# Kernel tuning notes

Measured on AMD Instinct MI355X. Metric: run time of the kernel, lower is better.

## Reference

```python
import jax, jax.numpy as jnp
import numpy as np

N = 10000      # nodes
E = 640000     # directed edges
D = 128        # feature width
C = 10         # classes
G = 64         # graphs in batch


def setup_inputs() -> dict:
    key = jax.random.key(0)
    ks = jax.random.split(key, 9)
    x = jax.random.normal(ks[0], (N, D), dtype=jnp.float32)
    edge_index = jax.random.randint(ks[1], (2, E), 0, N, dtype=jnp.int64)
    batch = jnp.sort(jax.random.randint(ks[2], (N,), 0, G, dtype=jnp.int64))
    scale = 1.0 / np.sqrt(D)
    W1 = jax.random.normal(ks[3], (D, D), dtype=jnp.float32) * scale
    W2 = jax.random.normal(ks[4], (D, D), dtype=jnp.float32) * scale
    W3 = jax.random.normal(ks[5], (D, D), dtype=jnp.float32) * scale
    W4 = jax.random.normal(ks[6], (D, D), dtype=jnp.float32) * scale
    fc_w = jax.random.normal(ks[7], (D, C), dtype=jnp.float32) * scale
    fc_b = jnp.zeros((C,), dtype=jnp.float32)
    return {"x": x, "edge_index": edge_index, "batch": batch,
            "W1": W1, "W2": W2, "W3": W3, "W4": W4,
            "fc_w": fc_w, "fc_b": fc_b}


def _gcn_conv(x, src, dst, deg_inv_sqrt, W):
    # GCNConv: h = x @ W; aggregate D^{-1/2}(A+I)D^{-1/2} h; then ReLU (activation).
    h = x @ W                                        # [N, D]
    norm = deg_inv_sqrt[src] * deg_inv_sqrt[dst]     # [E]
    msgs = h[src] * norm[:, None]                    # gather + scale
    agg = jax.ops.segment_sum(msgs, dst, num_segments=N)
    agg = agg + h * (deg_inv_sqrt * deg_inv_sqrt)[:, None]  # self-loop term
    return jax.nn.relu(agg)


def reference(x, edge_index, batch, W1, W2, W3, W4, fc_w, fc_b):
    src, dst = edge_index[0], edge_index[1]
    # degree counting self-loops (A + I normalization)
    deg = jax.ops.segment_sum(jnp.ones((E,), x.dtype), dst, num_segments=N) + 1.0
    deg_inv_sqrt = jax.lax.rsqrt(deg)
    for W in (W1, W2, W3, W4):
        x = _gcn_conv(x, src, dst, deg_inv_sqrt, W)
    xr = jax.ops.segment_sum(x, batch, num_segments=G)   # global_add_pool
    logits = x @ fc_w + fc_b
    return jax.nn.log_softmax(logits, axis=1), xr
```

## Files before the change

### kernel.cpp

```cpp
#include <hip/hip_runtime.h>
#include <hip/hip_fp16.h>
#include <math.h>

#define N_NODES 10000
#define N_EDGES 640000
#define DIM     128
#define NCLS    10
#define NGRAPH  64
#define NB      157
#define NBB     160
#define SEG     64
#define EPB     4000
#define NPB     8

typedef unsigned int uint32;
typedef unsigned short ushort16;
typedef _Float16 h2v __attribute__((ext_vector_type(2)));

#define SEL_LO 0x00003C00u
#define SEL_HI 0x3C000000u

__device__ __forceinline__ h2v as_h2(uint32 u) { h2v r; __builtin_memcpy(&r, &u, 4); return r; }

__device__ __forceinline__ float fd2(uint32 w, uint32 p, float acc) {
#if __has_builtin(__builtin_amdgcn_fdot2)
    return __builtin_amdgcn_fdot2(as_h2(w), as_h2(p), acc, false);
#else
    h2v a = as_h2(w), b = as_h2(p);
    return acc + (float)a[0] * (float)b[0] + (float)a[1] * (float)b[1];
#endif
}
__device__ __forceinline__ float f16lo(uint32 u) { return (float)as_h2(u)[0]; }
__device__ __forceinline__ float f16hi(uint32 u) { return (float)as_h2(u)[1]; }
__device__ __forceinline__ ushort16 f32_f16(float f) {
    return __half_as_ushort(__float2half(f));
}
__device__ __forceinline__ uint32 pack_f16x2(float lo, float hi) {
    __half2 h = __floats2half2_rn(lo, hi);
    uint32 u; __builtin_memcpy(&u, &h, 4); return u;
}

__global__ __launch_bounds__(256) void binA_gemm1(const int* __restrict__ src,
                                                  const int* __restrict__ dst,
                                                  int* __restrict__ cntG,
                                                  uint32* __restrict__ bins,
                                                  const float* __restrict__ X,
                                                  const float* __restrict__ W,
                                                  const float* __restrict__ W2,
                                                  const float* __restrict__ W3,
                                                  const float* __restrict__ W4,
                                                  uint32* __restrict__ Wp,
                                                  ushort16* __restrict__ Gh,
                                                  float* __restrict__ xr) {
    __shared__ uint32 pk[EPB];
    __shared__ int cntS[NB], offS[NB], curS[NB];

    if (blockIdx.x < 625) {
        int c    = threadIdx.x & 127;
        int rg   = threadIdx.x >> 7;
        int row0 = blockIdx.x * 16 + rg * 8;
        const float* xb = X + row0 * DIM;
        float acc[8] = {0.f, 0.f, 0.f, 0.f, 0.f, 0.f, 0.f, 0.f};
        for (int k = 0; k < DIM; k += 4) {
            float w0 = W[(k + 0) * DIM + c];
            float w1 = W[(k + 1) * DIM + c];
            float w2 = W[(k + 2) * DIM + c];
            float w3 = W[(k + 3) * DIM + c];
#pragma unroll
            for (int r = 0; r < 8; r++) {
                float4 xv = *(const float4*)(xb + r * DIM + k);
                acc[r] += xv.x * w0 + xv.y * w1 + xv.z * w2 + xv.w * w3;
            }
        }
#pragma unroll
        for (int r = 0; r < 8; r++)
            Gh[(row0 + r) * DIM + c] = f32_f16(acc[r]);
        return;
    }

    if (blockIdx.x >= 786) {
        int w = blockIdx.x - 786;
        const float* Ws = (w == 0) ? W2 : (w == 1) ? W3 : W4;
        uint32* Wd = Wp + w * (64 * DIM);
        for (int i = threadIdx.x; i < 64 * DIM; i += 256) {
            int k2 = i >> 7, c = i & 127;
            Wd[i] = pack_f16x2(Ws[(2 * k2) * DIM + c], Ws[(2 * k2 + 1) * DIM + c]);
        }
        return;
    }

    if (blockIdx.x == 785) {
        float4 z = make_float4(0.f, 0.f, 0.f, 0.f);
        for (int j = threadIdx.x; j < NGRAPH * DIM / 4; j += 256)
            ((float4*)xr)[j] = z;
        return;
    }

    int ab  = blockIdx.x - 625;
    int tid = threadIdx.x;
    for (int i = tid; i < NB; i += 256) cntS[i] = 0;
    __syncthreads();

    int base = ab * EPB;
    uint32 pr[16];
#pragma unroll
    for (int it = 0; it < 16; it++) {
        int i = it * 256 + tid;
        uint32 p = 0xffffffffu;
        if (i < EPB) {
            int e = base + i;
            p = ((uint32)dst[e] << 16) | (uint32)src[e];
            atomicAdd(&cntS[p >> 22], 1);
        }
        pr[it] = p;
    }
    __syncthreads();

    if (tid < 64) {
        int carry = 0;
        for (int r = 0; r < 3; r++) {
            int idx = r * 64 + tid;
            int v = (idx < NB) ? cntS[idx] : 0;
            int inc = v;
#pragma unroll
            for (int o = 1; o < 64; o <<= 1) {
                int u = __shfl_up(inc, o, 64);
                if (tid >= o) inc += u;
            }
            if (idx < NB) { offS[idx] = inc - v + carry; curS[idx] = inc - v + carry; }
            carry += __shfl(inc, 63, 64);
        }
    }
    __syncthreads();

#pragma unroll
    for (int it = 0; it < 16; it++) {
        uint32 p = pr[it];
        if (p != 0xffffffffu) {
            int b = p >> 22;
            pk[atomicAdd(&curS[b], 1)] = p;
        }
    }
    __syncthreads();

#pragma unroll
    for (int it = 0; it < 16; it++) {
        int i = it * 256 + tid;
        if (i < EPB) {
            uint32 u = pk[i];
            int b = u >> 22;
            int gp = i - offS[b];
            if (gp < SEG) bins[(size_t)(b * NBB + ab) * SEG + gp] = u;
        }
    }
    if (tid < NB) {
        int c = cntS[tid];
        cntG[tid * NBB + ab] = c < SEG ? c : SEG;
    }
}

__global__ __launch_bounds__(256) void binB2(const int* __restrict__ cntG,
                                             const uint32* __restrict__ bins,
                                             ushort16* __restrict__ col,
                                             int* __restrict__ deg,
                                             float* __restrict__ dis,
                                             ushort16* __restrict__ Gh) {
    __shared__ ushort16 adj[32 * 128];
    __shared__ int cnt2[32];
    __shared__ int segc[NBB];
    int b    = blockIdx.x >> 1;
    int half = blockIdx.x & 1;
    int tid  = threadIdx.x;
    if (tid < 32) cnt2[tid] = 0;
    if (tid < NBB) segc[tid] = cntG[b * NBB + tid];
    __syncthreads();

    const uint32* bb = bins + (size_t)b * NBB * SEG;
    for (int i = tid; i < NBB * SEG; i += 256) {
        int seg = i >> 6, idx = i & 63;
        if (idx < segc[seg]) {
            uint32 u = bb[i];
            int local = (u >> 16) & 63;
            if ((local >> 5) == half) {
                int l5 = local & 31;
                int r = atomicAdd(&cnt2[l5], 1);
                if (r < 128) adj[(l5 << 7) + r] = (ushort16)(u & 0xffffu);
            }
        }
    }
    __syncthreads();

    uint4* dstp = (uint4*)(col + (size_t)b * 64 * 128 + half * 32 * 128);
    const uint4* srcp = (const uint4*)adj;
    for (int j = tid; j < 512; j += 256) dstp[j] = srcp[j];
    if (tid < 32) {
        int node = b * 64 + half * 32 + tid;
        int c = cnt2[tid] < 128 ? cnt2[tid] : 128;
        deg[node] = c;
        dis[node] = rsqrtf((float)c + 1.0f);
    }

    uint4* Gh4 = (uint4*)Gh;
    int node0 = b * 64 + half * 32;
    for (int j = tid; j < 32 * 16; j += 256) {
        int rl = j >> 4, q = j & 15;
        if (node0 + rl >= N_NODES) continue;
        int c = cnt2[rl] < 128 ? cnt2[rl] : 128;
        float dv = rsqrtf((float)c + 1.0f);
        uint4 g = Gh4[(size_t)(node0 + rl) * 16 + q];
        g.x = pack_f16x2(f16lo(g.x) * dv, f16hi(g.x) * dv);
        g.y = pack_f16x2(f16lo(g.y) * dv, f16hi(g.y) * dv);
        g.z = pack_f16x2(f16lo(g.z) * dv, f16hi(g.z) * dv);
        g.w = pack_f16x2(f16lo(g.w) * dv, f16hi(g.w) * dv);
        Gh4[(size_t)(node0 + rl) * 16 + q] = g;
    }
}

template <bool PACK_OUT>
__device__ __forceinline__ void agg_to_lds(const ushort16* __restrict__ Gh,
                                           const int* __restrict__ deg,
                                           const ushort16* __restrict__ col,
                                           const float* __restrict__ dis,
                                           void* __restrict__ Xout) {
    int tid  = threadIdx.x;
    int wave = tid >> 6;
    int lane = tid & 63;
    int grp  = lane >> 4;
    int sl   = lane & 15;
    const uint32* g32 = (const uint32*)Gh;
    const uint32* gp  = g32 + (sl << 2);

#pragma unroll
    for (int i = 0; i < 2; i++) {
        int vr = wave * 2 + i;
        int v  = blockIdx.x * NPB + vr;
        int dv = deg[v];
        uint32 colpack = ((const uint32*)(col + ((size_t)v << 7)))[lane];
        float acc[8];
#pragma unroll
        for (int j = 0; j < 8; j++) acc[j] = 0.f;

        int kk = 0;
        for (; kk + 16 <= dv; kk += 16) {
            int k0 = kk + grp, k1 = kk + 4 + grp, k2 = kk + 8 + grp, k3 = kk + 12 + grp;
            uint32 cp0 = __shfl(colpack, k0 >> 1, 64);
            uint32 cp1 = __shfl(colpack, k1 >> 1, 64);
            uint32 cp2 = __shfl(colpack, k2 >> 1, 64);
            uint32 cp3 = __shfl(colpack, k3 >> 1, 64);
            int u0 = (k0 & 1) ? (int)(cp0 >> 16) : (int)(cp0 & 0xffffu);
            int u1 = (k1 & 1) ? (int)(cp1 >> 16) : (int)(cp1 & 0xffffu);
            int u2 = (k2 & 1) ? (int)(cp2 >> 16) : (int)(cp2 & 0xffffu);
            int u3 = (k3 & 1) ? (int)(cp3 >> 16) : (int)(cp3 & 0xffffu);
            uint4 w0 = *(const uint4*)(gp + (u0 << 6));
            uint4 w1 = *(const uint4*)(gp + (u1 << 6));
            uint4 w2 = *(const uint4*)(gp + (u2 << 6));
            uint4 w3 = *(const uint4*)(gp + (u3 << 6));
            acc[0] = fd2(w0.x, SEL_LO, acc[0]); acc[1] = fd2(w0.x, SEL_HI, acc[1]);
            acc[2] = fd2(w0.y, SEL_LO, acc[2]); acc[3] = fd2(w0.y, SEL_HI, acc[3]);
            acc[4] = fd2(w0.z, SEL_LO, acc[4]); acc[5] = fd2(w0.z, SEL_HI, acc[5]);
            acc[6] = fd2(w0.w, SEL_LO, acc[6]); acc[7] = fd2(w0.w, SEL_HI, acc[7]);
            acc[0] = fd2(w1.x, SEL_LO, acc[0]); acc[1] = fd2(w1.x, SEL_HI, acc[1]);
            acc[2] = fd2(w1.y, SEL_LO, acc[2]); acc[3] = fd2(w1.y, SEL_HI, acc[3]);
            acc[4] = fd2(w1.z, SEL_LO, acc[4]); acc[5] = fd2(w1.z, SEL_HI, acc[5]);
            acc[6] = fd2(w1.w, SEL_LO, acc[6]); acc[7] = fd2(w1.w, SEL_HI, acc[7]);
            acc[0] = fd2(w2.x, SEL_LO, acc[0]); acc[1] = fd2(w2.x, SEL_HI, acc[1]);
            acc[2] = fd2(w2.y, SEL_LO, acc[2]); acc[3] = fd2(w2.y, SEL_HI, acc[3]);
            acc[4] = fd2(w2.z, SEL_LO, acc[4]); acc[5] = fd2(w2.z, SEL_HI, acc[5]);
            acc[6] = fd2(w2.w, SEL_LO, acc[6]); acc[7] = fd2(w2.w, SEL_HI, acc[7]);
            acc[0] = fd2(w3.x, SEL_LO, acc[0]); acc[1] = fd2(w3.x, SEL_HI, acc[1]);
            acc[2] = fd2(w3.y, SEL_LO, acc[2]); acc[3] = fd2(w3.y, SEL_HI, acc[3]);
            acc[4] = fd2(w3.z, SEL_LO, acc[4]); acc[5] = fd2(w3.z, SEL_HI, acc[5]);
            acc[6] = fd2(w3.w, SEL_LO, acc[6]); acc[7] = fd2(w3.w, SEL_HI, acc[7]);
        }
        for (; kk + 8 <= dv; kk += 8) {
            int k0 = kk + grp, k1 = kk + 4 + grp;
            uint32 cp0 = __shfl(colpack, k0 >> 1, 64);
            uint32 cp1 = __shfl(colpack, k1 >> 1, 64);
            int u0 = (k0 & 1) ? (int)(cp0 >> 16) : (int)(cp0 & 0xffffu);
            int u1 = (k1 & 1) ? (int)(cp1 >> 16) : (int)(cp1 & 0xffffu);
            uint4 w0 = *(const uint4*)(gp + (u0 << 6));
            uint4 w1 = *(const uint4*)(gp + (u1 << 6));
            acc[0] = fd2(w0.x, SEL_LO, acc[0]); acc[1] = fd2(w0.x, SEL_HI, acc[1]);
            acc[2] = fd2(w0.y, SEL_LO, acc[2]); acc[3] = fd2(w0.y, SEL_HI, acc[3]);
            acc[4] = fd2(w0.z, SEL_LO, acc[4]); acc[5] = fd2(w0.z, SEL_HI, acc[5]);
            acc[6] = fd2(w0.w, SEL_LO, acc[6]); acc[7] = fd2(w0.w, SEL_HI, acc[7]);
            acc[0] = fd2(w1.x, SEL_LO, acc[0]); acc[1] = fd2(w1.x, SEL_HI, acc[1]);
            acc[2] = fd2(w1.y, SEL_LO, acc[2]); acc[3] = fd2(w1.y, SEL_HI, acc[3]);
            acc[4] = fd2(w1.z, SEL_LO, acc[4]); acc[5] = fd2(w1.z, SEL_HI, acc[5]);
            acc[6] = fd2(w1.w, SEL_LO, acc[6]); acc[7] = fd2(w1.w, SEL_HI, acc[7]);
        }
        for (; kk < dv; kk += 4) {
            int k = kk + grp;
            uint32 cp = __shfl(colpack, (k >> 1) & 63, 64);
            int u = (k & 1) ? (int)(cp >> 16) : (int)(cp & 0xffffu);
            if (k < dv) {
                uint4 w = *(const uint4*)(gp + (u << 6));
                acc[0] = fd2(w.x, SEL_LO, acc[0]); acc[1] = fd2(w.x, SEL_HI, acc[1]);
                acc[2] = fd2(w.y, SEL_LO, acc[2]); acc[3] = fd2(w.y, SEL_HI, acc[3]);
                acc[4] = fd2(w.z, SEL_LO, acc[4]); acc[5] = fd2(w.z, SEL_HI, acc[5]);
                acc[6] = fd2(w.w, SEL_LO, acc[6]); acc[7] = fd2(w.w, SEL_HI, acc[7]);
            }
        }
#pragma unroll
        for (int j = 0; j < 8; j++) {
            acc[j] += __shfl_xor(acc[j], 16, 64);
            acc[j] += __shfl_xor(acc[j], 32, 64);
        }
        float sv = dis[v];
        uint4 hs = *(const uint4*)(gp + (v << 6));
        float r0 = sv * (acc[0] + f16lo(hs.x));
        float r1 = sv * (acc[1] + f16hi(hs.x));
        float r2 = sv * (acc[2] + f16lo(hs.y));
        float r3 = sv * (acc[3] + f16hi(hs.y));
        float r4 = sv * (acc[4] + f16lo(hs.z));
        float r5 = sv * (acc[5] + f16hi(hs.z));
        float r6 = sv * (acc[6] + f16lo(hs.w));
        float r7 = sv * (acc[7] + f16hi(hs.w));
        if (grp == 0) {
            if (PACK_OUT) {
                uint32* o = (uint32*)Xout + vr * 64 + sl * 4;
                uint4 pk4;
                pk4.x = pack_f16x2(fmaxf(r0, 0.f), fmaxf(r1, 0.f));
                pk4.y = pack_f16x2(fmaxf(r2, 0.f), fmaxf(r3, 0.f));
                pk4.z = pack_f16x2(fmaxf(r4, 0.f), fmaxf(r5, 0.f));
                pk4.w = pack_f16x2(fmaxf(r6, 0.f), fmaxf(r7, 0.f));
                *(uint4*)o = pk4;
            } else {
                float4* o = (float4*)((float*)Xout + vr * DIM + sl * 8);
                o[0] = make_float4(fmaxf(r0, 0.f), fmaxf(r1, 0.f),
                                   fmaxf(r2, 0.f), fmaxf(r3, 0.f));
                o[1] = make_float4(fmaxf(r4, 0.f), fmaxf(r5, 0.f),
                                   fmaxf(r6, 0.f), fmaxf(r7, 0.f));
            }
        }
    }
}

__global__ __launch_bounds__(256) void fused_layer(const ushort16* __restrict__ Gh_in,
                                                   const int* __restrict__ deg,
                                                   const ushort16* __restrict__ col,
                                                   const float* __restrict__ dis,
                                                   const uint32* __restrict__ Wp,
                                                   ushort16* __restrict__ Gh_out) {
    __shared__ __align__(16) uint32 Xh[NPB * 64];
    agg_to_lds<true>(Gh_in, deg, col, dis, Xh);
    __syncthreads();

    int c  = threadIdx.x & 127;
    int rg = threadIdx.x >> 7;
    int row0 = blockIdx.x * NPB + rg * 4;
    const uint4* Xh4 = (const uint4*)Xh;
    float acc[4] = {0.f, 0.f, 0.f, 0.f};
    for (int q = 0; q < 16; q++) {
        uint32 wp0 = Wp[(4 * q + 0) * DIM + c];
        uint32 wp1 = Wp[(4 * q + 1) * DIM + c];
        uint32 wp2 = Wp[(4 * q + 2) * DIM + c];
        uint32 wp3 = Wp[(4 * q + 3) * DIM + c];
#pragma unroll
        for (int r = 0; r < 4; r++) {
            uint4 xv = Xh4[(rg * 4 + r) * 16 + q];
            acc[r] = fd2(xv.x, wp0, acc[r]);
            acc[r] = fd2(xv.y, wp1, acc[r]);
            acc[r] = fd2(xv.z, wp2, acc[r]);
            acc[r] = fd2(xv.w, wp3, acc[r]);
        }
    }
#pragma unroll
    for (int r = 0; r < 4; r++) {
        int row = row0 + r;
        Gh_out[row * DIM + c] = f32_f16(acc[r] * dis[row]);
    }
}

__global__ __launch_bounds__(256) void fused_last(const ushort16* __restrict__ Gh_in,
                                                  const int* __restrict__ deg,
                                                  const ushort16* __restrict__ col,
                                                  const float* __restrict__ dis,
                                                  const int* __restrict__ batch,
                                                  const float* __restrict__ fcw,
                                                  const float* __restrict__ fcb,
                                                  float* __restrict__ xr,
                                                  float* __restrict__ out) {
    __shared__ float Xs[NPB * DIM];
    agg_to_lds<false>(Gh_in, deg, col, dis, Xs);
    __syncthreads();

    int wave = threadIdx.x >> 6;
    int lane = threadIdx.x & 63;
#pragma unroll
    for (int i = 0; i < 2; i++) {
        int vr   = wave * 2 + i;
        int node = blockIdx.x * NPB + vr;
        float xl = Xs[vr * DIM + lane];
        float xh = Xs[vr * DIM + 64 + lane];
        float lg[NCLS];
#pragma unroll
        for (int c2 = 0; c2 < NCLS; c2++) {
            float p = xl * fcw[lane * NCLS + c2] + xh * fcw[(lane + 64) * NCLS + c2];
#pragma unroll
            for (int off = 32; off >= 1; off >>= 1) p += __shfl_xor(p, off, 64);
            lg[c2] = p + fcb[c2];
        }
        float m = lg[0];
#pragma unroll
        for (int c2 = 1; c2 < NCLS; c2++) m = fmaxf(m, lg[c2]);
        float s = 0.f;
#pragma unroll
        for (int c2 = 0; c2 < NCLS; c2++) s += expf(lg[c2] - m);
        float lse = m + logf(s);
        if (lane < NCLS) out[node * NCLS + lane] = lg[lane] - lse;
    }

    if (threadIdx.x < 128) {
        int start = blockIdx.x * NPB;
        int t = threadIdx.x;
        int b = batch[start];
        float a = 0.f;
        for (int n = 0; n < NPB; n++) {
            int bn = batch[start + n];
            if (bn != b) { atomicAdd(&xr[b * DIM + t], a); a = 0.f; b = bn; }
            a += Xs[n * DIM + t];
        }
        atomicAdd(&xr[b * DIM + t], a);
    }
}


extern "C" void kernel_launch(void* const* d_in, const int* in_sizes, int n_in,
                              void* d_out, int out_size, void* d_ws, size_t ws_size,
                              hipStream_t stream) {
    const float* x     = (const float*)d_in[0];
    const int*   ei    = (const int*)d_in[1];
    const int*   src   = ei;
    const int*   dst   = ei + N_EDGES;
    const int*   batch = (const int*)d_in[2];
    const float* W1    = (const float*)d_in[3];
    const float* W2    = (const float*)d_in[4];
    const float* W3    = (const float*)d_in[5];
    const float* W4    = (const float*)d_in[6];
    const float* fcw   = (const float*)d_in[7];
    const float* fcb   = (const float*)d_in[8];

    float* out_ls = (float*)d_out;
    float* out_xr = out_ls + N_NODES * NCLS;

    int*      cntG = (int*)d_ws;
    int*      deg  = cntG + NB * NBB;
    float*    dis  = (float*)(deg + 10240);
    uint32*   bins = (uint32*)(dis + 10240);
    ushort16* col  = (ushort16*)(bins + (size_t)NB * NBB * SEG);
    ushort16* Gh_a = col + (size_t)NB * 64 * 128;
    ushort16* Gh_b = Gh_a + (size_t)N_NODES * DIM;
    uint32*   Wp   = (uint32*)(Gh_b + (size_t)N_NODES * DIM);

    binA_gemm1<<<789, 256, 0, stream>>>(src, dst, cntG, bins, x, W1,
                                        W2, W3, W4, Wp, Gh_a, out_xr);
    binB2     <<<2 * NB, 256, 0, stream>>>(cntG, bins, col, deg, dis, Gh_a);

    fused_layer<<<N_NODES / NPB, 256, 0, stream>>>(Gh_a, deg, col, dis, Wp, Gh_b);
    fused_layer<<<N_NODES / NPB, 256, 0, stream>>>(Gh_b, deg, col, dis,
                                                   Wp + 64 * DIM, Gh_a);
    fused_layer<<<N_NODES / NPB, 256, 0, stream>>>(Gh_a, deg, col, dis,
                                                   Wp + 2 * 64 * DIM, Gh_b);
    fused_last <<<N_NODES / NPB, 256, 0, stream>>>(Gh_b, deg, col, dis, batch,
                                                   fcw, fcb, out_xr, out_ls);
}
```

Measured before the change: 190.4 us.

## Replace fixed per-block edge segments with global atomic cursor per bin

Edge binning previously wrote each binning block's edges into fixed 64-slot segments per destination bin, so the second pass scanned 160 sparse segments. Now each block reserves a contiguous range in the bin with an atomicAdd on a global cursor, and the second pass reads a dense, compacted list of edges. This cuts the scan and memory traffic in binB2 and drops the per-segment count array. It adds a memset launch and global atomics, and edges past the 4608-entry bin capacity are silently dropped.

```diff
diff --git a/kernel.cpp b/kernel.cpp
--- a/kernel.cpp
+++ b/kernel.cpp
@@ -8,8 +8,7 @@
 #define NCLS    10
 #define NGRAPH  64
 #define NB      157
-#define NBB     160
-#define SEG     64
+#define BCAP    4608
 #define EPB     4000
 #define NPB     8
 
@@ -42,7 +41,7 @@
 
 __global__ __launch_bounds__(256) void binA_gemm1(const int* __restrict__ src,
                                                   const int* __restrict__ dst,
-                                                  int* __restrict__ cntG,
+                                                  int* __restrict__ gcursor,
                                                   uint32* __restrict__ bins,
                                                   const float* __restrict__ X,
                                                   const float* __restrict__ W,
@@ -53,7 +52,7 @@
                                                   ushort16* __restrict__ Gh,
                                                   float* __restrict__ xr) {
     __shared__ uint32 pk[EPB];
-    __shared__ int cntS[NB], offS[NB], curS[NB];
+    __shared__ int cntS[NB], offS[NB], curS[NB], gposS[NB];
 
     if (blockIdx.x < 625) {
         int c    = threadIdx.x & 127;
@@ -143,23 +142,22 @@
     }
     __syncthreads();
 
+    if (tid < NB) gposS[tid] = atomicAdd(&gcursor[tid], cntS[tid]);
+    __syncthreads();
+
 #pragma unroll
     for (int it = 0; it < 16; it++) {
         int i = it * 256 + tid;
         if (i < EPB) {
             uint32 u = pk[i];
             int b = u >> 22;
-            int gp = i - offS[b];
-            if (gp < SEG) bins[(size_t)(b * NBB + ab) * SEG + gp] = u;
-        }
-    }
-    if (tid < NB) {
-        int c = cntS[tid];
-        cntG[tid * NBB + ab] = c < SEG ? c : SEG;
-    }
-}
-
-__global__ __launch_bounds__(256) void binB2(const int* __restrict__ cntG,
+            int gp = gposS[b] + (i - offS[b]);
+            if (gp < BCAP) bins[b * BCAP + gp] = u;
+        }
+    }
+}
+
+__global__ __launch_bounds__(256) void binB2(const int* __restrict__ gcursor,
                                              const uint32* __restrict__ bins,
                                              ushort16* __restrict__ col,
                                              int* __restrict__ deg,
@@ -167,29 +165,24 @@
                                              ushort16* __restrict__ Gh) {
     __shared__ ushort16 adj[32 * 128];
     __shared__ int cnt2[32];
-    __shared__ int segc[NBB];
     int b    = blockIdx.x >> 1;
     int half = blockIdx.x & 1;
     int tid  = threadIdx.x;
     if (tid < 32) cnt2[tid] = 0;
-    if (tid < NBB) segc[tid] = cntG[b * NBB + tid];
-    __syncthreads();
-
-    const uint32* bb = bins + (size_t)b * NBB * SEG;
-    for (int i = tid; i < NBB * SEG; i += 256) {
-        int seg = i >> 6, idx = i & 63;
-        if (idx < segc[seg]) {
-            uint32 u = bb[i];
-            int local = (u >> 16) & 63;
-            if ((local >> 5) == half) {
-                int l5 = local & 31;
-                int r = atomicAdd(&cnt2[l5], 1);
-                if (r < 128) adj[(l5 << 7) + r] = (ushort16)(u & 0xffffu);
-            }
-        }
-    }
-    __syncthreads();
-
+    __syncthreads();
+    int tc = gcursor[b];
+    if (tc > BCAP) tc = BCAP;
+    const uint32* bb = bins + b * BCAP;
+    for (int i = tid; i < tc; i += 256) {
+        uint32 u = bb[i];
+        int local = (u >> 16) & 63;
+        if ((local >> 5) == half) {
+            int l5 = local & 31;
+            int r = atomicAdd(&cnt2[l5], 1);
+            if (r < 128) adj[(l5 << 7) + r] = (ushort16)(u & 0xffffu);
+        }
+    }
+    __syncthreads();
     uint4* dstp = (uint4*)(col + (size_t)b * 64 * 128 + half * 32 * 128);
     const uint4* srcp = (const uint4*)adj;
     for (int j = tid; j < 512; j += 256) dstp[j] = srcp[j];
@@ -444,18 +437,20 @@
     float* out_ls = (float*)d_out;
     float* out_xr = out_ls + N_NODES * NCLS;
 
-    int*      cntG = (int*)d_ws;
-    int*      deg  = cntG + NB * NBB;
-    float*    dis  = (float*)(deg + 10240);
-    uint32*   bins = (uint32*)(dis + 10240);
-    ushort16* col  = (ushort16*)(bins + (size_t)NB * NBB * SEG);
-    ushort16* Gh_a = col + (size_t)NB * 64 * 128;
-    ushort16* Gh_b = Gh_a + (size_t)N_NODES * DIM;
-    uint32*   Wp   = (uint32*)(Gh_b + (size_t)N_NODES * DIM);
-
-    binA_gemm1<<<789, 256, 0, stream>>>(src, dst, cntG, bins, x, W1,
+    int*      gcursor = (int*)d_ws;
+    int*      deg     = gcursor + 256;
+    float*    dis     = (float*)(deg + 10240);
+    uint32*   bins    = (uint32*)(dis + 10240);
+    ushort16* col     = (ushort16*)(bins + NB * BCAP);
+    ushort16* Gh_a    = col + (size_t)NB * 64 * 128;
+    ushort16* Gh_b    = Gh_a + (size_t)N_NODES * DIM;
+    uint32*   Wp      = (uint32*)(Gh_b + (size_t)N_NODES * DIM);
+
+    hipMemsetAsync(gcursor, 0, 256 * sizeof(int), stream);
+
+    binA_gemm1<<<789, 256, 0, stream>>>(src, dst, gcursor, bins, x, W1,
                                         W2, W3, W4, Wp, Gh_a, out_xr);
-    binB2     <<<2 * NB, 256, 0, stream>>>(cntG, bins, col, deg, dis, Gh_a);
+    binB2     <<<2 * NB, 256, 0, stream>>>(gcursor, bins, col, deg, dis, Gh_a);
 
     fused_layer<<<N_NODES / NPB, 256, 0, stream>>>(Gh_a, deg, col, dis, Wp, Gh_b);
     fused_layer<<<N_NODES / NPB, 256, 0, stream>>>(Gh_b, deg, col, dis,
```

After: 181.7 us, median of 2. 1.05x faster.

## Store binned edges densely per block with offsets instead of fixed-size padded segments

Applied to the files above, without the earlier changes.

The binning stage now writes each block's locally sorted edge list contiguously and records per-bucket offsets, replacing fixed 64-slot padded segments per bucket with separate counts. The second binning kernel reads each source block's range from those offsets, with one thread per source segment looping serially. This cuts workspace size and stops dropping edges when a bucket overflows, but the serial per-thread loops in binB2 may be less parallel than the old strided read.

```diff
diff --git a/kernel.cpp b/kernel.cpp
--- a/kernel.cpp
+++ b/kernel.cpp
@@ -9,8 +9,8 @@
 #define NGRAPH  64
 #define NB      157
 #define NBB     160
-#define SEG     64
 #define EPB     4000
+#define OSTR    160
 #define NPB     8
 
 typedef unsigned int uint32;
@@ -42,7 +42,7 @@
 
 __global__ __launch_bounds__(256) void binA_gemm1(const int* __restrict__ src,
                                                   const int* __restrict__ dst,
-                                                  int* __restrict__ cntG,
+                                                  int* __restrict__ offG,
                                                   uint32* __restrict__ bins,
                                                   const float* __restrict__ X,
                                                   const float* __restrict__ W,
@@ -146,20 +146,13 @@
 #pragma unroll
     for (int it = 0; it < 16; it++) {
         int i = it * 256 + tid;
-        if (i < EPB) {
-            uint32 u = pk[i];
-            int b = u >> 22;
-            int gp = i - offS[b];
-            if (gp < SEG) bins[(size_t)(b * NBB + ab) * SEG + gp] = u;
-        }
-    }
-    if (tid < NB) {
-        int c = cntS[tid];
-        cntG[tid * NBB + ab] = c < SEG ? c : SEG;
-    }
-}
-
-__global__ __launch_bounds__(256) void binB2(const int* __restrict__ cntG,
+        if (i < EPB) bins[ab * EPB + i] = pk[i];
+    }
+    if (tid < NB)  offG[ab * OSTR + tid] = offS[tid];
+    if (tid == NB) offG[ab * OSTR + NB]  = EPB;
+}
+
+__global__ __launch_bounds__(256) void binB2(const int* __restrict__ offG,
                                              const uint32* __restrict__ bins,
                                              ushort16* __restrict__ col,
                                              int* __restrict__ deg,
@@ -167,19 +160,18 @@
                                              ushort16* __restrict__ Gh) {
     __shared__ ushort16 adj[32 * 128];
     __shared__ int cnt2[32];
-    __shared__ int segc[NBB];
     int b    = blockIdx.x >> 1;
     int half = blockIdx.x & 1;
     int tid  = threadIdx.x;
     if (tid < 32) cnt2[tid] = 0;
-    if (tid < NBB) segc[tid] = cntG[b * NBB + tid];
-    __syncthreads();
-
-    const uint32* bb = bins + (size_t)b * NBB * SEG;
-    for (int i = tid; i < NBB * SEG; i += 256) {
-        int seg = i >> 6, idx = i & 63;
-        if (idx < segc[seg]) {
-            uint32 u = bb[i];
+    __syncthreads();
+
+    if (tid < NBB) {
+        int s = offG[tid * OSTR + b];
+        int e = offG[tid * OSTR + b + 1];
+        const uint32* seg = bins + tid * EPB;
+        for (int i = s; i < e; i++) {
+            uint32 u = seg[i];
             int local = (u >> 16) & 63;
             if ((local >> 5) == half) {
                 int l5 = local & 31;
@@ -444,18 +436,18 @@
     float* out_ls = (float*)d_out;
     float* out_xr = out_ls + N_NODES * NCLS;
 
-    int*      cntG = (int*)d_ws;
-    int*      deg  = cntG + NB * NBB;
+    int*      offG = (int*)d_ws;
+    int*      deg  = offG + NBB * OSTR;
     float*    dis  = (float*)(deg + 10240);
     uint32*   bins = (uint32*)(dis + 10240);
-    ushort16* col  = (ushort16*)(bins + (size_t)NB * NBB * SEG);
+    ushort16* col  = (ushort16*)(bins + NBB * EPB);
     ushort16* Gh_a = col + (size_t)NB * 64 * 128;
     ushort16* Gh_b = Gh_a + (size_t)N_NODES * DIM;
     uint32*   Wp   = (uint32*)(Gh_b + (size_t)N_NODES * DIM);
 
-    binA_gemm1<<<789, 256, 0, stream>>>(src, dst, cntG, bins, x, W1,
+    binA_gemm1<<<789, 256, 0, stream>>>(src, dst, offG, bins, x, W1,
                                         W2, W3, W4, Wp, Gh_a, out_xr);
-    binB2     <<<2 * NB, 256, 0, stream>>>(cntG, bins, col, deg, dis, Gh_a);
+    binB2     <<<2 * NB, 256, 0, stream>>>(offG, bins, col, deg, dis, Gh_a);
 
     fused_layer<<<N_NODES / NPB, 256, 0, stream>>>(Gh_a, deg, col, dis, Wp, Gh_b);
     fused_layer<<<N_NODES / NPB, 256, 0, stream>>>(Gh_b, deg, col, dis,
```

Result: no change. 189.4 us (-0.6%).
